# Kernel optimization log

Hardware: AMD Instinct MI355X
Metric: run time of the kernel (lower is better)

## Reference

```python
import jax, jax.numpy as jnp
import numpy as np

EPS = 1e-5
NI = 33  # 1 dense row + sparse_inp_proj_dim (32) rows
TRIL_I, TRIL_J = np.tril_indices(NI, k=-1)  # 528 pairs, row-major like torch.tril_indices


def layer_norm(x, g, b):
    m = jnp.mean(x, axis=-1, keepdims=True)
    v = jnp.mean(jnp.square(x - m), axis=-1, keepdims=True)
    return (x - m) * jax.lax.rsqrt(v + EPS) * g + b


def setup_inputs() -> dict:
    key = jax.random.key(0)
    ks = jax.random.split(key, 8)
    B, D_DENSE, N_SP, D_SP = 32768, 256, 26, 64
    E, PROJ, MAXD, NFLAT = 128, 32, 512, 528
    dense_t = jax.random.normal(ks[0], (B, D_DENSE), dtype=jnp.float32)
    sparse_t = jax.random.normal(ks[1], (B, N_SP, D_SP), dtype=jnp.float32)
    # LazyLinear weights (bias=False because use_layernorm=True)
    Wd = jax.random.normal(ks[2], (E, D_DENSE), dtype=jnp.float32) / np.sqrt(D_DENSE)
    Ws = jax.random.normal(ks[3], (E, D_SP), dtype=jnp.float32) / np.sqrt(D_SP)
    Wsi = jax.random.normal(ks[4], (PROJ, N_SP), dtype=jnp.float32) / np.sqrt(N_SP)
    Wl = jax.random.normal(ks[5], (MAXD, NFLAT), dtype=jnp.float32) / np.sqrt(NFLAT)
    gd = jnp.ones((E,), jnp.float32); bd = jnp.zeros((E,), jnp.float32)
    gs = jnp.ones((E,), jnp.float32); bs = jnp.zeros((E,), jnp.float32)
    gsi = jnp.ones((PROJ,), jnp.float32); bsi = jnp.zeros((PROJ,), jnp.float32)
    gl = jnp.ones((MAXD,), jnp.float32); bl = jnp.zeros((MAXD,), jnp.float32)
    return {"dense_t": dense_t, "sparse_t": sparse_t, "Wd": Wd, "gd": gd, "bd": bd,
            "Ws": Ws, "gs": gs, "bs": bs, "Wsi": Wsi, "gsi": gsi, "bsi": bsi,
            "Wl": Wl, "gl": gl, "bl": bl, "dims_in_use": 384}


def reference(dense_t, sparse_t, Wd, gd, bd, Ws, gs, bs, Wsi, gsi, bsi, Wl, gl, bl, dims_in_use):
    # dense projection to embedding_dim + LN
    x = layer_norm(dense_t @ Wd.T, gd, bd)                       # [B, 128]
    # sparse projection to embedding_dim + LN
    y = layer_norm(jnp.einsum('bnd,ed->bne', sparse_t, Ws), gs, bs)  # [B, 26, 128]
    # project sparse rows 26 -> 32 (applied on transposed layout) + LN
    y = jnp.einsum('bne,pn->bep', y, Wsi)                        # [B, 128, 32]
    y = layer_norm(y, gsi, bsi)
    y = jnp.swapaxes(y, 1, 2)                                    # [B, 32, 128]
    T = jnp.concatenate([x[:, None, :], y], axis=1)              # [B, 33, 128]
    Z = jnp.einsum('bnd,bmd->bnm', T, T)                         # [B, 33, 33]
    Zflat = Z[:, TRIL_I, TRIL_J]                                 # [B, 528]
    out = layer_norm(Zflat @ Wl.T, gl, bl)                       # [B, 512]
    maxd = out.shape[-1]
    mask = (jnp.arange(maxd) < dims_in_use).astype(out.dtype)
    return out * mask
```

## Files before the change

### kernel.cpp

```cpp
#include <hip/hip_runtime.h>
#include <hip/hip_bf16.h>
#include <math.h>

#define EPS 1e-5f

typedef __attribute__((ext_vector_type(8))) short short8v;
typedef __attribute__((ext_vector_type(4))) short short4v;
typedef __attribute__((ext_vector_type(4))) float f32x4;
typedef __attribute__((ext_vector_type(2))) unsigned uint2v;
typedef __attribute__((ext_vector_type(4))) unsigned uint4v;

__device__ __forceinline__ short f2bf(float f) {
    union { float f; unsigned u; } v; v.f = f;
    unsigned r = v.u + 0x7FFFu + ((v.u >> 16) & 1u);
    return (short)(r >> 16);
}
__device__ __forceinline__ unsigned cvt_pk(float lo, float hi) {
    unsigned r;
    asm("v_cvt_pk_bf16_f32 %0, %1, %2" : "=v"(r) : "v"(lo), "v"(hi));
    return r;
}
__device__ __forceinline__ short8v pack8(float4 a, float4 b) {
    union { uint4v u; short8v s; } cv;
    cv.u = (uint4v){ cvt_pk(a.x, a.y), cvt_pk(a.z, a.w),
                     cvt_pk(b.x, b.y), cvt_pk(b.z, b.w) };
    return cv.s;
}

__global__ __launch_bounds__(256) void k_prep(
    const float* __restrict__ Ws, const float* __restrict__ Wsi,
    const float* __restrict__ Wl, const float* __restrict__ Wd,
    short* __restrict__ wsb, short* __restrict__ wsib, short* __restrict__ wlb,
    short* __restrict__ wdb)
{
    int i = blockIdx.x * 256 + threadIdx.x;
    if (i < 128 * 64) wsb[i] = f2bf(Ws[i]);
    if (i < 32 * 32) { int p = i >> 5, n = i & 31; wsib[i] = (n < 26) ? f2bf(Wsi[p * 26 + n]) : (short)0; }
    if (i < 128 * 256) wdb[i] = f2bf(Wd[i]);
    if (i < 512 * 544) { int c = i / 544, k = i - c * 544; wlb[i] = (k < 528) ? f2bf(Wl[c * 528 + k]) : (short)0; }
}

__global__ __launch_bounds__(256) void k_dense_ln(
    const float* __restrict__ dense, const short* __restrict__ wdb,
    const float* __restrict__ gd, const float* __restrict__ bd,
    short* __restrict__ xbf)
{
    __shared__ float red[4][32][2];
    __shared__ float minv[32][2];
    const int t = threadIdx.x;
    const int wv = t >> 6, l = t & 63;
    const int g = l >> 4, c = l & 15;
    const size_t r0 = (size_t)blockIdx.x * 32;

    f32x4 acc[2][2];
    #pragma unroll
    for (int mt = 0; mt < 2; ++mt)
        #pragma unroll
        for (int nt = 0; nt < 2; ++nt) acc[mt][nt] = (f32x4){0.f, 0.f, 0.f, 0.f};

    #pragma unroll
    for (int ks = 0; ks < 8; ++ks) {
        short8v b0 = *(const short8v*)(wdb + (wv * 32 + c) * 256 + ks * 32 + g * 8);
        short8v b1 = *(const short8v*)(wdb + (wv * 32 + 16 + c) * 256 + ks * 32 + g * 8);
        #pragma unroll
        for (int mt = 0; mt < 2; ++mt) {
            const float* p = dense + (r0 + mt * 16 + c) * 256 + ks * 32 + g * 8;
            short8v a = pack8(*(const float4*)p, *(const float4*)(p + 4));
            acc[mt][0] = __builtin_amdgcn_mfma_f32_16x16x32_bf16(a, b0, acc[mt][0], 0, 0, 0);
            acc[mt][1] = __builtin_amdgcn_mfma_f32_16x16x32_bf16(a, b1, acc[mt][1], 0, 0, 0);
        }
    }
    #pragma unroll
    for (int mt = 0; mt < 2; ++mt)
        #pragma unroll
        for (int reg = 0; reg < 4; ++reg) {
            float v0 = acc[mt][0][reg], v1 = acc[mt][1][reg];
            float s = v0 + v1, q = v0 * v0 + v1 * v1;
            s += __shfl_xor(s, 1); q += __shfl_xor(q, 1);
            s += __shfl_xor(s, 2); q += __shfl_xor(q, 2);
            s += __shfl_xor(s, 4); q += __shfl_xor(q, 4);
            s += __shfl_xor(s, 8); q += __shfl_xor(q, 8);
            if (c == 0) {
                red[wv][mt * 16 + g * 4 + reg][0] = s;
                red[wv][mt * 16 + g * 4 + reg][1] = q;
            }
        }
    __syncthreads();
    if (t < 32) {
        float S = red[0][t][0] + red[1][t][0] + red[2][t][0] + red[3][t][0];
        float Q = red[0][t][1] + red[1][t][1] + red[2][t][1] + red[3][t][1];
        float m = S * (1.f / 128.f);
        float v = Q * (1.f / 128.f) - m * m;
        minv[t][0] = m; minv[t][1] = rsqrtf(v + EPS);
    }
    __syncthreads();
    const float ge0 = gd[wv * 32 + c],      be0 = bd[wv * 32 + c];
    const float ge1 = gd[wv * 32 + 16 + c], be1 = bd[wv * 32 + 16 + c];
    #pragma unroll
    for (int mt = 0; mt < 2; ++mt)
        #pragma unroll
        for (int reg = 0; reg < 4; ++reg) {
            int rr = mt * 16 + g * 4 + reg;
            float m = minv[rr][0], inv = minv[rr][1];
            xbf[(r0 + rr) * 128 + wv * 32 + c]      = f2bf((acc[mt][0][reg] - m) * inv * ge0 + be0);
            xbf[(r0 + rr) * 128 + wv * 32 + 16 + c] = f2bf((acc[mt][1][reg] - m) * inv * ge1 + be1);
        }
}

__global__ __launch_bounds__(64, 4) void k_middle(
    const float* __restrict__ sparse, const short* __restrict__ Wsb,
    const float* __restrict__ gs, const float* __restrict__ bs,
    const short* __restrict__ Wsib, const float* __restrict__ gsi, const float* __restrict__ bsi,
    const short* __restrict__ xbf, short* __restrict__ zf)
{
    __shared__ __align__(16) short W[4224];
    const int l = threadIdx.x;
    const int g = l >> 4;
    const int c = l & 15;
    const size_t row = (size_t)blockIdx.x;

    short8v afr[2][2];
    #pragma unroll
    for (int mt = 0; mt < 2; ++mt) {
        const int n = mt * 16 + c;
        #pragma unroll
        for (int ks = 0; ks < 2; ++ks) {
            if (n < 26) {
                const float* p = sparse + row * 1664 + n * 64 + ks * 32 + g * 8;
                afr[mt][ks] = pack8(*(const float4*)p, *(const float4*)(p + 4));
            } else {
                afr[mt][ks] = (short8v){0, 0, 0, 0, 0, 0, 0, 0};
            }
        }
    }
    short8v xrow = *(const short8v*)(xbf + row * 128 + c * 8);

    f32x4 acc[2][8];
    #pragma unroll
    for (int mt = 0; mt < 2; ++mt)
        #pragma unroll
        for (int nt = 0; nt < 8; ++nt) acc[mt][nt] = (f32x4){0.f, 0.f, 0.f, 0.f};
    #pragma unroll
    for (int nt = 0; nt < 8; ++nt) {
        short8v b0 = *(const short8v*)(Wsb + (nt * 16 + c) * 64 + g * 8);
        short8v b1 = *(const short8v*)(Wsb + (nt * 16 + c) * 64 + 32 + g * 8);
        #pragma unroll
        for (int mt = 0; mt < 2; ++mt) {
            acc[mt][nt] = __builtin_amdgcn_mfma_f32_16x16x32_bf16(afr[mt][0], b0, acc[mt][nt], 0, 0, 0);
            acc[mt][nt] = __builtin_amdgcn_mfma_f32_16x16x32_bf16(afr[mt][1], b1, acc[mt][nt], 0, 0, 0);
        }
    }
    float m_[2][4], inv_[2][4];
    #pragma unroll
    for (int mt = 0; mt < 2; ++mt)
        #pragma unroll
        for (int reg = 0; reg < 4; ++reg) {
            float s = 0.f, q = 0.f;
            #pragma unroll
            for (int nt = 0; nt < 8; ++nt) { float v = acc[mt][nt][reg]; s += v; q += v * v; }
            s += __shfl_xor(s, 1); q += __shfl_xor(q, 1);
            s += __shfl_xor(s, 2); q += __shfl_xor(q, 2);
            s += __shfl_xor(s, 4); q += __shfl_xor(q, 4);
            s += __shfl_xor(s, 8); q += __shfl_xor(q, 8);
            float m = s * (1.f / 128.f);
            float v = q * (1.f / 128.f) - m * m;
            m_[mt][reg] = m; inv_[mt][reg] = rsqrtf(v + EPS);
        }
    #pragma unroll
    for (int mt = 0; mt < 2; ++mt)
        #pragma unroll
        for (int nt = 0; nt < 8; ++nt) {
            float ge = gs[nt * 16 + c], be = bs[nt * 16 + c];
            float v0 = 0.f, v1 = 0.f, v2 = 0.f, v3 = 0.f;
            {
                int n0 = mt * 16 + g * 4;
                float a0 = (acc[mt][nt][0] - m_[mt][0]) * inv_[mt][0] * ge + be;
                float a1 = (acc[mt][nt][1] - m_[mt][1]) * inv_[mt][1] * ge + be;
                float a2 = (acc[mt][nt][2] - m_[mt][2]) * inv_[mt][2] * ge + be;
                float a3 = (acc[mt][nt][3] - m_[mt][3]) * inv_[mt][3] * ge + be;
                v0 = (n0 + 0 < 26) ? a0 : 0.f;
                v1 = (n0 + 1 < 26) ? a1 : 0.f;
                v2 = (n0 + 2 < 26) ? a2 : 0.f;
                v3 = (n0 + 3 < 26) ? a3 : 0.f;
            }
            union { uint2v u; short4v s; } yv;
            yv.u = (uint2v){ cvt_pk(v0, v1), cvt_pk(v2, v3) };
            int e = nt * 16 + c;
            int gi = 2 * mt + (g >> 1);
            int off = e * 32 + ((gi ^ ((e >> 1) & 3)) << 3) + (g & 1) * 4;
            *(short4v*)(W + off) = yv.s;
        }
    __syncthreads();

    short8v awsi0 = *(const short8v*)(Wsib + c * 32 + g * 8);
    short8v awsi1 = *(const short8v*)(Wsib + (16 + c) * 32 + g * 8);
    float gsiA[4], bsiA[4], gsiB[4], bsiB[4];
    #pragma unroll
    for (int reg = 0; reg < 4; ++reg) {
        gsiA[reg] = gsi[g * 4 + reg];      bsiA[reg] = bsi[g * 4 + reg];
        gsiB[reg] = gsi[16 + g * 4 + reg]; bsiB[reg] = bsi[16 + g * 4 + reg];
    }
    short8v tv[8];
    #pragma unroll
    for (int mt = 0; mt < 8; ++mt) {
        int e = mt * 16 + c;
        short8v bf = *(const short8v*)(W + e * 32 + ((g ^ ((e >> 1) & 3)) << 3));
        f32x4 c0 = (f32x4){0, 0, 0, 0}, c1 = (f32x4){0, 0, 0, 0};
        c0 = __builtin_amdgcn_mfma_f32_16x16x32_bf16(awsi0, bf, c0, 0, 0, 0);
        c1 = __builtin_amdgcn_mfma_f32_16x16x32_bf16(awsi1, bf, c1, 0, 0, 0);
        float s = 0.f, q = 0.f;
        #pragma unroll
        for (int reg = 0; reg < 4; ++reg) {
            float v0 = c0[reg], v1 = c1[reg];
            s += v0 + v1; q += v0 * v0 + v1 * v1;
        }
        s += __shfl_xor(s, 16); q += __shfl_xor(q, 16);
        s += __shfl_xor(s, 32); q += __shfl_xor(q, 32);
        float m = s * (1.f / 32.f);
        float var = q * (1.f / 32.f) - m * m;
        float inv = rsqrtf(var + EPS);
        float a0 = (c0[0] - m) * inv * gsiA[0] + bsiA[0];
        float a1 = (c0[1] - m) * inv * gsiA[1] + bsiA[1];
        float a2 = (c0[2] - m) * inv * gsiA[2] + bsiA[2];
        float a3 = (c0[3] - m) * inv * gsiA[3] + bsiA[3];
        float b0 = (c1[0] - m) * inv * gsiB[0] + bsiB[0];
        float b1 = (c1[1] - m) * inv * gsiB[1] + bsiB[1];
        float b2 = (c1[2] - m) * inv * gsiB[2] + bsiB[2];
        float b3 = (c1[3] - m) * inv * gsiB[3] + bsiB[3];
        union { uint4v u; short8v s8; } cv;
        cv.u = (uint4v){ cvt_pk(a0, a1), cvt_pk(a2, a3), cvt_pk(b0, b1), cvt_pk(b2, b3) };
        tv[mt] = cv.s8;
    }
    __syncthreads();

    if (l < 16) *(short8v*)(W + l * 8) = xrow;
    #pragma unroll
    for (int mt = 0; mt < 8; ++mt) {
        int d = mt * 16 + c;
        #pragma unroll
        for (int reg = 0; reg < 4; ++reg) {
            int i0 = 1 + g * 4 + reg;
            int i1 = 17 + g * 4 + reg;
            W[i0 * 128 + (d ^ ((i0 & 7) << 3))] = tv[mt][reg];
            W[i1 * 128 + (d ^ ((i1 & 7) << 3))] = tv[mt][4 + reg];
        }
    }
    __syncthreads();

    f32x4 z00 = (f32x4){0,0,0,0}, z10 = (f32x4){0,0,0,0}, z11 = (f32x4){0,0,0,0};
    f32x4 z20 = (f32x4){0,0,0,0}, z21 = (f32x4){0,0,0,0};
    #pragma unroll
    for (int ks = 0; ks < 4; ++ks) {
        int d = ks * 32 + g * 8;
        short8v f0 = *(const short8v*)(W + c * 128 + (d ^ ((c & 7) << 3)));
        short8v f1 = *(const short8v*)(W + (16 + c) * 128 + (d ^ ((c & 7) << 3)));
        short8v f2 = *(const short8v*)(W + 32 * 128 + d);
        z00 = __builtin_amdgcn_mfma_f32_16x16x32_bf16(f0, f0, z00, 0, 0, 0);
        z10 = __builtin_amdgcn_mfma_f32_16x16x32_bf16(f1, f0, z10, 0, 0, 0);
        z11 = __builtin_amdgcn_mfma_f32_16x16x32_bf16(f1, f1, z11, 0, 0, 0);
        z20 = __builtin_amdgcn_mfma_f32_16x16x32_bf16(f2, f0, z20, 0, 0, 0);
        z21 = __builtin_amdgcn_mfma_f32_16x16x32_bf16(f2, f1, z21, 0, 0, 0);
    }
    short* zr = zf + row * 544;
    #pragma unroll
    for (int reg = 0; reg < 4; ++reg) {
        int i0 = g * 4 + reg;
        { int i = i0;      int j = c;      if (j < i)  zr[i * (i - 1) / 2 + j] = f2bf(z00[reg]); }
        { int i = 16 + i0; int j = c;                  zr[i * (i - 1) / 2 + j] = f2bf(z10[reg]); }
        { int i = 16 + i0; int j = 16 + c; if (j < i)  zr[i * (i - 1) / 2 + j] = f2bf(z11[reg]); }
        { int i = 32 + i0; int j = c;      if (i < 33) zr[i * (i - 1) / 2 + j] = f2bf(z20[reg]); }
        { int i = 32 + i0; int j = 16 + c; if (i < 33) zr[i * (i - 1) / 2 + j] = f2bf(z21[reg]); }
    }
    if (l < 16) zr[528 + l] = 0;
}

__global__ __launch_bounds__(512) void k_final(
    const short* __restrict__ zf, const short* __restrict__ Wlb,
    const float* __restrict__ gl, const float* __restrict__ bl,
    const int* __restrict__ dims_p, float* __restrict__ out)
{
    __shared__ __align__(16) short zlds[32][552];
    __shared__ __align__(16) short wlds[512][40];
    __shared__ float red[32][4][2];
    const int t = threadIdx.x;
    const int wv = t >> 6;
    const int l = t & 63;
    const int g = l >> 4, c = l & 15;
    const int wm = wv >> 2;
    const int wn = wv & 3;
    const size_t r0 = (size_t)blockIdx.x * 32;

    for (int f = t; f < 32 * 68; f += 512) {
        int r = f / 68, s = f - r * 68;
        *(short8v*)(&zlds[r][s * 8]) = *(const short8v*)(zf + (r0 + r) * 544 + s * 8);
    }
    short8v wreg[4];
    #pragma unroll
    for (int j = 0; j < 4; ++j) {
        int f = t + j * 512, cc = f >> 2, part = f & 3;
        wreg[j] = *(const short8v*)(Wlb + cc * 544 + part * 8);
    }
    f32x4 acc[8];
    #pragma unroll
    for (int i = 0; i < 8; ++i) acc[i] = (f32x4){0, 0, 0, 0};
    for (int ks = 0; ks < 17; ++ks) {
        __syncthreads();
        #pragma unroll
        for (int j = 0; j < 4; ++j) {
            int f = t + j * 512, cc = f >> 2, part = f & 3;
            *(short8v*)(&wlds[cc][part * 8]) = wreg[j];
        }
        if (ks < 16) {
            #pragma unroll
            for (int j = 0; j < 4; ++j) {
                int f = t + j * 512, cc = f >> 2, part = f & 3;
                wreg[j] = *(const short8v*)(Wlb + cc * 544 + (ks + 1) * 32 + part * 8);
            }
        }
        __syncthreads();
        short8v af = *(const short8v*)(&zlds[wm * 16 + c][ks * 32 + g * 8]);
        #pragma unroll
        for (int nt = 0; nt < 8; ++nt) {
            short8v bf = *(const short8v*)(&wlds[wn * 128 + nt * 16 + c][g * 8]);
            acc[nt] = __builtin_amdgcn_mfma_f32_16x16x32_bf16(af, bf, acc[nt], 0, 0, 0);
        }
    }
    #pragma unroll
    for (int reg = 0; reg < 4; ++reg) {
        float s = 0.f, q = 0.f;
        #pragma unroll
        for (int nt = 0; nt < 8; ++nt) { float v = acc[nt][reg]; s += v; q += v * v; }
        s += __shfl_xor(s, 1); q += __shfl_xor(q, 1);
        s += __shfl_xor(s, 2); q += __shfl_xor(q, 2);
        s += __shfl_xor(s, 4); q += __shfl_xor(q, 4);
        s += __shfl_xor(s, 8); q += __shfl_xor(q, 8);
        if (c == 0) { red[wm * 16 + g * 4 + reg][wn][0] = s; red[wm * 16 + g * 4 + reg][wn][1] = q; }
    }
    __syncthreads();
    const int dims = dims_p[0];
    float M[4], INV[4];
    #pragma unroll
    for (int reg = 0; reg < 4; ++reg) {
        int rr = wm * 16 + g * 4 + reg;
        float S = red[rr][0][0] + red[rr][1][0] + red[rr][2][0] + red[rr][3][0];
        float Q = red[rr][0][1] + red[rr][1][1] + red[rr][2][1] + red[rr][3][1];
        float m = S * (1.f / 512.f);
        float v = Q * (1.f / 512.f) - m * m;
        M[reg] = m; INV[reg] = rsqrtf(v + EPS);
    }
    #pragma unroll
    for (int nt = 0; nt < 8; ++nt) {
        int cc = wn * 128 + nt * 16 + c;
        float gg = (cc < dims) ? gl[cc] : 0.f;
        float bb = (cc < dims) ? bl[cc] : 0.f;
        #pragma unroll
        for (int reg = 0; reg < 4; ++reg) {
            int rr = wm * 16 + g * 4 + reg;
            out[(r0 + rr) * 512 + cc] = (acc[nt][reg] - M[reg]) * INV[reg] * gg + bb;
        }
    }
}

extern "C" void kernel_launch(void* const* d_in, const int* in_sizes, int n_in,
                              void* d_out, int out_size, void* d_ws, size_t ws_size,
                              hipStream_t stream)
{
    const float* dense  = (const float*)d_in[0];
    const float* sparse = (const float*)d_in[1];
    const float* Wd  = (const float*)d_in[2];
    const float* gd  = (const float*)d_in[3];
    const float* bd  = (const float*)d_in[4];
    const float* Ws  = (const float*)d_in[5];
    const float* gs  = (const float*)d_in[6];
    const float* bs  = (const float*)d_in[7];
    const float* Wsi = (const float*)d_in[8];
    const float* gsi = (const float*)d_in[9];
    const float* bsi = (const float*)d_in[10];
    const float* Wl  = (const float*)d_in[11];
    const float* gl  = (const float*)d_in[12];
    const float* bl  = (const float*)d_in[13];
    const int*   dims = (const int*)d_in[14];
    float* out = (float*)d_out;
    (void)n_in; (void)out_size; (void)ws_size;

    const int B = in_sizes[0] / 256;
    short* xbf = (short*)d_ws;
    short* zfw = xbf + (size_t)B * 128;
    short* wsb = zfw + (size_t)B * 544;
    short* wsib = wsb + 128 * 64;
    short* wlb  = wsib + 32 * 32;
    short* wdb  = wlb + 512 * 544;

    hipLaunchKernelGGL(k_prep, dim3(1088), dim3(256), 0, stream,
                       Ws, Wsi, Wl, Wd, wsb, wsib, wlb, wdb);
    hipLaunchKernelGGL(k_dense_ln, dim3(B / 32), dim3(256), 0, stream,
                       dense, wdb, gd, bd, xbf);
    hipLaunchKernelGGL(k_middle, dim3(B), dim3(64), 0, stream,
                       sparse, wsb, gs, bs, wsib, gsi, bsi, xbf, zfw);
    hipLaunchKernelGGL(k_final, dim3(B / 32), dim3(512), 0, stream,
                       zfw, wlb, gl, bl, dims, out);
}
```

Measured before the change: 224.1 us.

## Use truncating bf16 packing, add setprio around MFMA blocks, simplify row masking

Replaces the hardware round-to-nearest bf16 pack instruction with plain bit truncation when converting dense and sparse inputs and the intermediate layer-norm outputs. Wraps the MFMA loops in s_setprio raises so matrix work gets scheduling priority across waves. Replaces the per-element row-validity selects with a precomputed multiplicative mask that applies only to the second row tile. Truncation adds rounding bias that may hurt accuracy, and the conversions are likely a small share of the runtime in this memory-heavy kernel.

```diff
diff --git a/kernel.cpp b/kernel.cpp
--- a/kernel.cpp
+++ b/kernel.cpp
@@ -15,15 +15,14 @@
     unsigned r = v.u + 0x7FFFu + ((v.u >> 16) & 1u);
     return (short)(r >> 16);
 }
-__device__ __forceinline__ unsigned cvt_pk(float lo, float hi) {
-    unsigned r;
-    asm("v_cvt_pk_bf16_f32 %0, %1, %2" : "=v"(r) : "v"(lo), "v"(hi));
-    return r;
-}
-__device__ __forceinline__ short8v pack8(float4 a, float4 b) {
+__device__ __forceinline__ unsigned trunc2(float lo, float hi) {
+    union { float f; unsigned u; } a, b; a.f = lo; b.f = hi;
+    return (b.u & 0xFFFF0000u) | (a.u >> 16);
+}
+__device__ __forceinline__ short8v pack8t(float4 a, float4 b) {
     union { uint4v u; short8v s; } cv;
-    cv.u = (uint4v){ cvt_pk(a.x, a.y), cvt_pk(a.z, a.w),
-                     cvt_pk(b.x, b.y), cvt_pk(b.z, b.w) };
+    cv.u = (uint4v){ trunc2(a.x, a.y), trunc2(a.z, a.w),
+                     trunc2(b.x, b.y), trunc2(b.z, b.w) };
     return cv.s;
 }
 
@@ -65,7 +64,7 @@
         #pragma unroll
         for (int mt = 0; mt < 2; ++mt) {
             const float* p = dense + (r0 + mt * 16 + c) * 256 + ks * 32 + g * 8;
-            short8v a = pack8(*(const float4*)p, *(const float4*)(p + 4));
+            short8v a = pack8t(*(const float4*)p, *(const float4*)(p + 4));
             acc[mt][0] = __builtin_amdgcn_mfma_f32_16x16x32_bf16(a, b0, acc[mt][0], 0, 0, 0);
             acc[mt][1] = __builtin_amdgcn_mfma_f32_16x16x32_bf16(a, b1, acc[mt][1], 0, 0, 0);
         }
@@ -127,19 +126,23 @@
         for (int ks = 0; ks < 2; ++ks) {
             if (n < 26) {
                 const float* p = sparse + row * 1664 + n * 64 + ks * 32 + g * 8;
-                afr[mt][ks] = pack8(*(const float4*)p, *(const float4*)(p + 4));
+                afr[mt][ks] = pack8t(*(const float4*)p, *(const float4*)(p + 4));
             } else {
                 afr[mt][ks] = (short8v){0, 0, 0, 0, 0, 0, 0, 0};
             }
         }
     }
     short8v xrow = *(const short8v*)(xbf + row * 128 + c * 8);
+    float msk1[4];
+    #pragma unroll
+    for (int reg = 0; reg < 4; ++reg) msk1[reg] = (16 + g * 4 + reg < 26) ? 1.f : 0.f;
 
     f32x4 acc[2][8];
     #pragma unroll
     for (int mt = 0; mt < 2; ++mt)
         #pragma unroll
         for (int nt = 0; nt < 8; ++nt) acc[mt][nt] = (f32x4){0.f, 0.f, 0.f, 0.f};
+    __builtin_amdgcn_s_setprio(1);
     #pragma unroll
     for (int nt = 0; nt < 8; ++nt) {
         short8v b0 = *(const short8v*)(Wsb + (nt * 16 + c) * 64 + g * 8);
@@ -150,6 +153,7 @@
             acc[mt][nt] = __builtin_amdgcn_mfma_f32_16x16x32_bf16(afr[mt][1], b1, acc[mt][nt], 0, 0, 0);
         }
     }
+    __builtin_amdgcn_s_setprio(0);
     float m_[2][4], inv_[2][4];
     #pragma unroll
     for (int mt = 0; mt < 2; ++mt)
@@ -171,20 +175,13 @@
         #pragma unroll
         for (int nt = 0; nt < 8; ++nt) {
             float ge = gs[nt * 16 + c], be = bs[nt * 16 + c];
-            float v0 = 0.f, v1 = 0.f, v2 = 0.f, v3 = 0.f;
-            {
-                int n0 = mt * 16 + g * 4;
-                float a0 = (acc[mt][nt][0] - m_[mt][0]) * inv_[mt][0] * ge + be;
-                float a1 = (acc[mt][nt][1] - m_[mt][1]) * inv_[mt][1] * ge + be;
-                float a2 = (acc[mt][nt][2] - m_[mt][2]) * inv_[mt][2] * ge + be;
-                float a3 = (acc[mt][nt][3] - m_[mt][3]) * inv_[mt][3] * ge + be;
-                v0 = (n0 + 0 < 26) ? a0 : 0.f;
-                v1 = (n0 + 1 < 26) ? a1 : 0.f;
-                v2 = (n0 + 2 < 26) ? a2 : 0.f;
-                v3 = (n0 + 3 < 26) ? a3 : 0.f;
-            }
+            float a0 = (acc[mt][nt][0] - m_[mt][0]) * inv_[mt][0] * ge + be;
+            float a1 = (acc[mt][nt][1] - m_[mt][1]) * inv_[mt][1] * ge + be;
+            float a2 = (acc[mt][nt][2] - m_[mt][2]) * inv_[mt][2] * ge + be;
+            float a3 = (acc[mt][nt][3] - m_[mt][3]) * inv_[mt][3] * ge + be;
+            if (mt == 1) { a0 *= msk1[0]; a1 *= msk1[1]; a2 *= msk1[2]; a3 *= msk1[3]; }
             union { uint2v u; short4v s; } yv;
-            yv.u = (uint2v){ cvt_pk(v0, v1), cvt_pk(v2, v3) };
+            yv.u = (uint2v){ trunc2(a0, a1), trunc2(a2, a3) };
             int e = nt * 16 + c;
             int gi = 2 * mt + (g >> 1);
             int off = e * 32 + ((gi ^ ((e >> 1) & 3)) << 3) + (g & 1) * 4;
@@ -206,8 +203,10 @@
         int e = mt * 16 + c;
         short8v bf = *(const short8v*)(W + e * 32 + ((g ^ ((e >> 1) & 3)) << 3));
         f32x4 c0 = (f32x4){0, 0, 0, 0}, c1 = (f32x4){0, 0, 0, 0};
+        __builtin_amdgcn_s_setprio(1);
         c0 = __builtin_amdgcn_mfma_f32_16x16x32_bf16(awsi0, bf, c0, 0, 0, 0);
         c1 = __builtin_amdgcn_mfma_f32_16x16x32_bf16(awsi1, bf, c1, 0, 0, 0);
+        __builtin_amdgcn_s_setprio(0);
         float s = 0.f, q = 0.f;
         #pragma unroll
         for (int reg = 0; reg < 4; ++reg) {
@@ -228,7 +227,7 @@
         float b2 = (c1[2] - m) * inv * gsiB[2] + bsiB[2];
         float b3 = (c1[3] - m) * inv * gsiB[3] + bsiB[3];
         union { uint4v u; short8v s8; } cv;
-        cv.u = (uint4v){ cvt_pk(a0, a1), cvt_pk(a2, a3), cvt_pk(b0, b1), cvt_pk(b2, b3) };
+        cv.u = (uint4v){ trunc2(a0, a1), trunc2(a2, a3), trunc2(b0, b1), trunc2(b2, b3) };
         tv[mt] = cv.s8;
     }
     __syncthreads();
@@ -249,6 +248,7 @@
 
     f32x4 z00 = (f32x4){0,0,0,0}, z10 = (f32x4){0,0,0,0}, z11 = (f32x4){0,0,0,0};
     f32x4 z20 = (f32x4){0,0,0,0}, z21 = (f32x4){0,0,0,0};
+    __builtin_amdgcn_s_setprio(1);
     #pragma unroll
     for (int ks = 0; ks < 4; ++ks) {
         int d = ks * 32 + g * 8;
@@ -261,6 +261,7 @@
         z20 = __builtin_amdgcn_mfma_f32_16x16x32_bf16(f2, f0, z20, 0, 0, 0);
         z21 = __builtin_amdgcn_mfma_f32_16x16x32_bf16(f2, f1, z21, 0, 0, 0);
     }
+    __builtin_amdgcn_s_setprio(0);
     short* zr = zf + row * 544;
     #pragma unroll
     for (int reg = 0; reg < 4; ++reg) {
```

Result: slower. 242.8 us (+8.4%).
